# Kernel tuning notes

Measured on AMD Instinct MI355X. Metric: run time of the kernel, lower is better.

## Reference

```python
import jax, jax.numpy as jnp
import numpy as np

NUM_LAYERS = 4
OPTIONS = 32
SHAPE = (3, 32, 32)
D = int(np.prod(SHAPE))  # 3072
H = 256
B = 256


def setup_inputs() -> dict:
    key = jax.random.key(0)
    ks = jax.random.split(key, 4)
    inputs = jax.random.normal(ks[0], (B,) + SHAPE, dtype=jnp.float32)
    Wb = jax.random.normal(ks[1], (D, H), dtype=jnp.float32) * 0.02
    bb = jnp.zeros((H,), dtype=jnp.float32)
    Wo_stack = jax.random.normal(ks[2], (NUM_LAYERS, H, OPTIONS * D), dtype=jnp.float32) * 0.02
    bo_stack = jnp.zeros((NUM_LAYERS, OPTIONS * D), dtype=jnp.float32)
    bias_stack = jnp.zeros((NUM_LAYERS, OPTIONS, D), dtype=jnp.float32)
    return {"inputs": inputs, "Wb": Wb, "bb": bb, "Wo_stack": Wo_stack,
            "bo_stack": bo_stack, "bias_stack": bias_stack}


def reference(inputs, Wb, bb, Wo_stack, bo_stack, bias_stack):
    """Iterative residual vector quantization (VQ-DRAW encoder).

    Returns (encodings [B, num_layers] int32, reconstructions [B, *SHAPE]).
    """
    b = inputs.shape[0]
    x = inputs.reshape(b, D)                      # [B, D] flattened target
    cur = jnp.zeros_like(x)                       # current reconstruction
    encodings = []
    for i in range(NUM_LAYERS):
        base_out = jax.nn.relu(cur @ Wb + bb)                     # [B, H]
        layer_out = (base_out @ Wo_stack[i] + bo_stack[i])        # [B, O*D]
        layer_out = layer_out.reshape(b, OPTIONS, D) + bias_stack[i][None]
        new = cur[:, None, :] + layer_out                          # [B, O, D]
        # per-(example, option) MSE-sum loss, fused argmin over options
        losses = jnp.sum(jnp.square(new - x[:, None, :]), axis=-1)  # [B, O]
        idx = jnp.argmin(losses, axis=-1)                          # [B]
        encodings.append(idx)
        cur = jnp.take_along_axis(new, idx[:, None, None], axis=1)[:, 0]  # [B, D]
    return jnp.stack(encodings, axis=-1), cur.reshape(inputs.shape)
```

## Files before the change

kernel.cpp:

```cpp
#include <hip/hip_runtime.h>
#include <hip/hip_bf16.h>

#define B_ 256
#define D_ 3072
#define H_ 256
#define OPT_ 32
#define OD_ 98304
#define NL_ 4

typedef __attribute__((ext_vector_type(8))) short short8;
typedef __attribute__((ext_vector_type(4))) float f32x4;

__device__ __forceinline__ unsigned short f2bf(float f) {
    unsigned int u = __float_as_uint(f);
    unsigned int r = (u + 0x7FFFu + ((u >> 16) & 1u)) >> 16;
    return (unsigned short)r;
}

__global__ __launch_bounds__(256) void init_kernel(const float* __restrict__ x,
                                                   float* __restrict__ cur,
                                                   float* __restrict__ rx,
                                                   float* __restrict__ zpart) {
    int gid0 = blockIdx.x * 256 + threadIdx.x;
    for (int g = gid0; g < B_ * D_; g += 131072) {
        cur[g] = 0.f;
        rx[g] = -x[g];
    }
    for (int g = gid0; g < 16 * B_ * H_; g += 131072) zpart[g] = 0.f;
}

__global__ __launch_bounds__(256) void gemm1_kernel(const float* __restrict__ cur,
                                                    const float* __restrict__ Wb,
                                                    float* __restrict__ zpart) {
    int t = threadIdx.x;
    int ks = blockIdx.x >> 5;
    int bg = blockIdx.x & 31;
    const float* wp = Wb + (size_t)ks * 192 * H_ + t;
    const float* cp = cur + (size_t)(bg * 8) * D_ + ks * 192;
    float acc[8] = {0.f, 0.f, 0.f, 0.f, 0.f, 0.f, 0.f, 0.f};
#pragma unroll 4
    for (int dd = 0; dd < 192; ++dd) {
        float w = wp[(size_t)dd * H_];
#pragma unroll
        for (int g = 0; g < 8; ++g) acc[g] += cp[(size_t)g * D_ + dd] * w;
    }
#pragma unroll
    for (int g = 0; g < 8; ++g)
        zpart[ks * (B_ * H_) + (bg * 8 + g) * H_ + t] = acc[g];
}

__global__ __launch_bounds__(256) void e_kernel(const float* __restrict__ zpart,
                                                const float* __restrict__ bb,
                                                unsigned char* __restrict__ base_ready,
                                                float* __restrict__ basef) {
    int m = blockIdx.x, k = threadIdx.x;
    float z = bb[k];
#pragma unroll
    for (int ks = 0; ks < 16; ++ks) z += zpart[ks * (B_ * H_) + m * H_ + k];
    z = z > 0.f ? z : 0.f;
    *(unsigned short*)(base_ready + (k >> 5) * 20480 + m * 80 + (k & 31) * 2) = f2bf(z);
    basef[m * H_ + k] = z;
}

__global__ __launch_bounds__(512, 4) void g2_kernel(const unsigned char* __restrict__ base_ready,
                                                    const float* __restrict__ Wo,
                                                    const float* __restrict__ biasL,
                                                    const float* __restrict__ boL,
                                                    const float* __restrict__ rx,
                                                    float* __restrict__ partial) {
    __shared__ __align__(16) unsigned char ldsA[2][20480];
    __shared__ __align__(16) unsigned char ldsW[2][10240];

    int t = threadIdx.x;
    int lane = t & 63, wv = t >> 6;
    int bx = blockIdx.x;
    int ncol0 = bx * 128;
    int o = bx / 24;
    int dbase = (bx % 24) * 128;

    int wm = wv >> 1, wn = wv & 1;
    int lrow = lane & 15, lk = lane >> 4;
    int nW = t & 127, kq = t >> 7;

    f32x4 acc[4][4];
#pragma unroll
    for (int mi = 0; mi < 4; ++mi)
#pragma unroll
        for (int ni = 0; ni < 4; ++ni) acc[mi][ni] = 0.f;

    uint4 pa0, pa1, pa2;
    float wf[8];

#define LOADA(S) { const unsigned char* gA = base_ready + (S) * 20480;           \
    pa0 = *(const uint4*)(gA + t * 16);                                          \
    pa1 = *(const uint4*)(gA + 8192 + t * 16);                                   \
    if (t < 256) pa2 = *(const uint4*)(gA + 16384 + t * 16); }

#define LOADW(S) {                                                               \
    const float* gp0 = Wo + (size_t)((S) * 32 + kq * 4) * OD_ + ncol0 + nW;      \
    wf[0] = gp0[0]; wf[1] = gp0[OD_]; wf[2] = gp0[2 * OD_]; wf[3] = gp0[3 * OD_];\
    const float* gp1 = gp0 + (size_t)16 * OD_;                                   \
    wf[4] = gp1[0]; wf[5] = gp1[OD_]; wf[6] = gp1[2 * OD_]; wf[7] = gp1[3 * OD_]; }

#define WRITEA(BUF) {                                                            \
    *(uint4*)(ldsA[BUF] + t * 16) = pa0;                                         \
    *(uint4*)(ldsA[BUF] + 8192 + t * 16) = pa1;                                  \
    if (t < 256) *(uint4*)(ldsA[BUF] + 16384 + t * 16) = pa2; }

#define WRITEW(BUF) {                                                            \
    uint2 pk0, pk1;                                                              \
    pk0.x = (unsigned)f2bf(wf[0]) | ((unsigned)f2bf(wf[1]) << 16);               \
    pk0.y = (unsigned)f2bf(wf[2]) | ((unsigned)f2bf(wf[3]) << 16);               \
    *(uint2*)(ldsW[BUF] + nW * 80 + kq * 8) = pk0;                               \
    pk1.x = (unsigned)f2bf(wf[4]) | ((unsigned)f2bf(wf[5]) << 16);               \
    pk1.y = (unsigned)f2bf(wf[6]) | ((unsigned)f2bf(wf[7]) << 16);               \
    *(uint2*)(ldsW[BUF] + nW * 80 + 32 + kq * 8) = pk1; }

    LOADA(0); LOADW(0);
    WRITEA(0); WRITEW(0);
    __syncthreads();
    LOADA(1); LOADW(1);

    for (int s = 0; s < 8; ++s) {
        int cur = s & 1;
        short8 bfr[4];
#pragma unroll
        for (int ni = 0; ni < 4; ++ni) {
            int nn = wn * 64 + ni * 16 + lrow;
            bfr[ni] = *(const short8*)(ldsW[cur] + nn * 80 + lk * 16);
        }
#pragma unroll
        for (int mi = 0; mi < 4; ++mi) {
            int row = wm * 64 + mi * 16 + lrow;
            short8 af = *(const short8*)(ldsA[cur] + row * 80 + lk * 16);
#pragma unroll
            for (int ni = 0; ni < 4; ++ni)
                acc[mi][ni] = __builtin_amdgcn_mfma_f32_16x16x32_bf16(af, bfr[ni], acc[mi][ni], 0, 0, 0);
        }
        if (s < 7) { WRITEA(cur ^ 1); WRITEW(cur ^ 1); }
        __syncthreads();
        if (s < 6) { LOADA(s + 2); LOADW(s + 2); }
    }

#undef LOADA
#undef LOADW
#undef WRITEA
#undef WRITEW

    float q[4];
#pragma unroll
    for (int ni = 0; ni < 4; ++ni) {
        int dcol = dbase + wn * 64 + ni * 16 + lrow;
        q[ni] = biasL[o * D_ + dcol] + boL[o * D_ + dcol];
    }
    float ssum[4][4];
#pragma unroll
    for (int mi = 0; mi < 4; ++mi)
#pragma unroll
        for (int r = 0; r < 4; ++r) ssum[mi][r] = 0.f;

#pragma unroll
    for (int mi = 0; mi < 4; ++mi) {
#pragma unroll
        for (int ni = 0; ni < 4; ++ni) {
            int dcol = dbase + wn * 64 + ni * 16 + lrow;
#pragma unroll
            for (int r = 0; r < 4; ++r) {
                int rowm = wm * 64 + mi * 16 + lk * 4 + r;
                float tv = acc[mi][ni][r] + rx[rowm * D_ + dcol] + q[ni];
                ssum[mi][r] += tv * tv;
            }
        }
    }
#pragma unroll
    for (int mi = 0; mi < 4; ++mi)
#pragma unroll
        for (int r = 0; r < 4; ++r) {
            float v = ssum[mi][r];
            v += __shfl_xor(v, 1);
            v += __shfl_xor(v, 2);
            v += __shfl_xor(v, 4);
            v += __shfl_xor(v, 8);
            if (lrow == 0) {
                int rowm = wm * 64 + mi * 16 + lk * 4 + r;
                partial[(rowm * OPT_ + o) * 48 + (bx % 24) * 2 + wn] = v;
            }
        }
}

__global__ __launch_bounds__(256) void c_kernel(const float* __restrict__ partial,
                                                int* __restrict__ idxbuf,
                                                float* __restrict__ enc, int layer) {
    __shared__ float ls[32];
    int b = blockIdx.x, t = threadIdx.x;
    int oo = t >> 3, j8 = t & 7;
    const float* pp = partial + (b * OPT_ + oo) * 48;
    float v = 0.f;
#pragma unroll
    for (int j = 0; j < 6; ++j) v += pp[j8 + 8 * j];
    v += __shfl_xor(v, 1);
    v += __shfl_xor(v, 2);
    v += __shfl_xor(v, 4);
    if (j8 == 0) ls[oo] = v;
    __syncthreads();
    if (t < 32) {
        float mv = ls[t];
        int mi = t;
#pragma unroll
        for (int m = 16; m >= 1; m >>= 1) {
            float ov = __shfl_xor(mv, m);
            int oi = __shfl_xor(mi, m);
            if (ov < mv || (ov == mv && oi < mi)) { mv = ov; mi = oi; }
        }
        if (t == 0) {
            idxbuf[b] = mi;
            enc[b * NL_ + layer] = (float)mi;
        }
    }
}

__global__ __launch_bounds__(256) void bucket_kernel(const int* __restrict__ idxbuf,
                                                     int* __restrict__ ocount,
                                                     int* __restrict__ olist,
                                                     int* __restrict__ work) {
    __shared__ int lcnt[32];
    int t = threadIdx.x;
    if (t < 32) lcnt[t] = 0;
    __syncthreads();
    int o = idxbuf[t];
    int pos = atomicAdd(&lcnt[o], 1);
    olist[o * 256 + pos] = t;
    __syncthreads();
    if (t < 32) ocount[t] = lcnt[t];
    if (t == 0) {
        int n = 0;
        for (int oo = 0; oo < 32; ++oo) {
            int c = lcnt[oo];
            for (int ch = 0; ch * 8 < c; ++ch) work[n++] = (oo << 8) | ch;
        }
        work[63] = n;
    }
}

__global__ __launch_bounds__(256) void d_kernel(const int* __restrict__ work,
                                                const int* __restrict__ ocount,
                                                const int* __restrict__ olist,
                                                const float* __restrict__ basef,
                                                const float* __restrict__ Wo,
                                                const float* __restrict__ boL,
                                                const float* __restrict__ biasL,
                                                const float* __restrict__ x,
                                                float* __restrict__ cur,
                                                float* __restrict__ rx) {
    __shared__ float basL[8][256];
    int t = threadIdx.x;
    int dt = blockIdx.y;
    int nit = work[63];

    for (int j = blockIdx.x; j < nit; j += 32) {
        int wi = work[j];
        int o = wi >> 8;
        int c0 = (wi & 255) * 8;
        int cnt = ocount[o];
        int rem = cnt - c0;
        if (rem > 8) rem = 8;

        int bidx[8];
#pragma unroll
        for (int g = 0; g < 8; ++g) {
            int idx = c0 + g;
            if (idx >= cnt) idx = cnt - 1;
            bidx[g] = olist[o * 256 + idx];
        }
        __syncthreads();
#pragma unroll
        for (int g = 0; g < 8; ++g) basL[g][t] = basef[bidx[g] * H_ + t];
        __syncthreads();

        int d = dt * 256 + t;
        const float* wp = Wo + (size_t)o * D_ + d;
        size_t nn = (size_t)o * D_ + d;
        float bov = boL[nn];
        float biv = biasL[nn];

        float acc[8] = {0.f, 0.f, 0.f, 0.f, 0.f, 0.f, 0.f, 0.f};
        for (int k0 = 0; k0 < 256; k0 += 8) {
            float w[8];
#pragma unroll
            for (int u = 0; u < 8; ++u) w[u] = wp[(size_t)(k0 + u) * OD_];
#pragma unroll
            for (int h = 0; h < 2; ++h) {
                int kb = k0 + h * 4;
                f32x4 bv[8];
#pragma unroll
                for (int g = 0; g < 8; ++g) bv[g] = *(const f32x4*)&basL[g][kb];
#pragma unroll
                for (int u = 0; u < 4; ++u) {
                    float wu = w[h * 4 + u];
#pragma unroll
                    for (int g = 0; g < 8; ++g) acc[g] += bv[g][u] * wu;
                }
            }
        }
#pragma unroll
        for (int g = 0; g < 8; ++g) {
            if (g < rem) {
                int b = bidx[g];
                float outv = cur[b * D_ + d] + acc[g] + bov + biv;
                cur[b * D_ + d] = outv;
                rx[b * D_ + d] = outv - x[b * D_ + d];
            }
        }
    }
}

extern "C" void kernel_launch(void* const* d_in, const int* in_sizes, int n_in,
                              void* d_out, int out_size, void* d_ws, size_t ws_size,
                              hipStream_t stream) {
    const float* x    = (const float*)d_in[0];
    const float* Wb   = (const float*)d_in[1];
    const float* bb   = (const float*)d_in[2];
    const float* Wo   = (const float*)d_in[3];
    const float* bo   = (const float*)d_in[4];
    const float* bias = (const float*)d_in[5];

    float* out = (float*)d_out;
    float* enc = out;
    float* cur = out + 1024;

    float* ws = (float*)d_ws;
    float* zpart   = ws;
    float* partial = ws + 1048576;
    float* rx      = ws + 1441792;
    float* basef   = ws + 2228224;
    unsigned char* base_ready = (unsigned char*)(ws + 2293760);
    int* idxbuf    = (int*)(ws + 2334720);
    int* ocount    = (int*)(ws + 2334976);
    int* olist     = (int*)(ws + 2335008);
    int* work      = (int*)(ws + 2343200);

    init_kernel<<<512, 256, 0, stream>>>(x, cur, rx, zpart);

    for (int i = 0; i < NL_; ++i) {
        const float* WoL   = Wo + (size_t)i * H_ * OD_;
        const float* boLp  = bo + (size_t)i * OD_;
        const float* biasL = bias + (size_t)i * OD_;
        if (i > 0) gemm1_kernel<<<512, 256, 0, stream>>>(cur, Wb, zpart);
        e_kernel<<<256, 256, 0, stream>>>(zpart, bb, base_ready, basef);
        g2_kernel<<<768, 512, 0, stream>>>(base_ready, WoL, biasL, boLp, rx, partial);
        c_kernel<<<256, 256, 0, stream>>>(partial, idxbuf, enc, i);
        bucket_kernel<<<1, 256, 0, stream>>>(idxbuf, ocount, olist, work);
        d_kernel<<<dim3(32, 12), 256, 0, stream>>>(work, ocount, olist, basef, WoL, boLp, biasL, x, cur, rx);
    }
}
```

Baseline: 419.0 us.

## Use global_load_lds DMA in g2 pipeline and fold bucketing into d_kernel

The g2 GEMM now loads the A tile straight into LDS with global_load_lds instead of staging it through registers. It also double-buffers the W prefetch two stages ahead and uses explicit waitcnt/barrier placement, so loads overlap MFMA work. Separately, bucket_kernel is removed: each d_kernel block recomputes option counts and ranks from idxbuf in shared memory, saving one launch per layer. The cost is redundant bucketing work in every d block, extra syncs, and more reliance on hand-written waitcnt counts being correct.

Result: slower. 460.9 us (+10.0%).

```diff
diff --git a/kernel.cpp b/kernel.cpp
--- a/kernel.cpp
+++ b/kernel.cpp
@@ -88,41 +88,55 @@
 #pragma unroll
         for (int ni = 0; ni < 4; ++ni) acc[mi][ni] = 0.f;
 
-    uint4 pa0, pa1, pa2;
-    float wf[8];
-
-#define LOADA(S) { const unsigned char* gA = base_ready + (S) * 20480;           \
-    pa0 = *(const uint4*)(gA + t * 16);                                          \
-    pa1 = *(const uint4*)(gA + 8192 + t * 16);                                   \
-    if (t < 256) pa2 = *(const uint4*)(gA + 16384 + t * 16); }
-
-#define LOADW(S) {                                                               \
-    const float* gp0 = Wo + (size_t)((S) * 32 + kq * 4) * OD_ + ncol0 + nW;      \
-    wf[0] = gp0[0]; wf[1] = gp0[OD_]; wf[2] = gp0[2 * OD_]; wf[3] = gp0[3 * OD_];\
-    const float* gp1 = gp0 + (size_t)16 * OD_;                                   \
-    wf[4] = gp1[0]; wf[5] = gp1[OD_]; wf[6] = gp1[2 * OD_]; wf[7] = gp1[3 * OD_]; }
-
-#define WRITEA(BUF) {                                                            \
-    *(uint4*)(ldsA[BUF] + t * 16) = pa0;                                         \
-    *(uint4*)(ldsA[BUF] + 8192 + t * 16) = pa1;                                  \
-    if (t < 256) *(uint4*)(ldsA[BUF] + 16384 + t * 16) = pa2; }
-
-#define WRITEW(BUF) {                                                            \
-    uint2 pk0, pk1;                                                              \
-    pk0.x = (unsigned)f2bf(wf[0]) | ((unsigned)f2bf(wf[1]) << 16);               \
-    pk0.y = (unsigned)f2bf(wf[2]) | ((unsigned)f2bf(wf[3]) << 16);               \
-    *(uint2*)(ldsW[BUF] + nW * 80 + kq * 8) = pk0;                               \
-    pk1.x = (unsigned)f2bf(wf[4]) | ((unsigned)f2bf(wf[5]) << 16);               \
-    pk1.y = (unsigned)f2bf(wf[6]) | ((unsigned)f2bf(wf[7]) << 16);               \
+    float wfX[8], wfY[8];
+
+#define DMA_A(S, BUF) {                                                                  \
+    const unsigned char* gA = base_ready + (S) * 20480;                                  \
+    __builtin_amdgcn_global_load_lds(                                                    \
+        (const __attribute__((address_space(1))) unsigned int*)(gA + t * 16),            \
+        (__attribute__((address_space(3))) unsigned int*)(&ldsA[BUF][0] + wv * 1024),    \
+        16, 0, 0);                                                                       \
+    __builtin_amdgcn_global_load_lds(                                                    \
+        (const __attribute__((address_space(1))) unsigned int*)(gA + 8192 + t * 16),     \
+        (__attribute__((address_space(3))) unsigned int*)(&ldsA[BUF][0] + 8192 + wv * 1024), \
+        16, 0, 0);                                                                       \
+    if (wv < 4)                                                                          \
+        __builtin_amdgcn_global_load_lds(                                                \
+            (const __attribute__((address_space(1))) unsigned int*)(gA + 16384 + t * 16),\
+            (__attribute__((address_space(3))) unsigned int*)(&ldsA[BUF][0] + 16384 + wv * 1024), \
+            16, 0, 0); }
+
+#define LOADW_(S, WF) {                                                                  \
+    const float* gp0 = Wo + (size_t)((S) * 32 + kq * 4) * OD_ + ncol0 + nW;              \
+    WF[0] = gp0[0]; WF[1] = gp0[OD_]; WF[2] = gp0[2 * OD_]; WF[3] = gp0[3 * OD_];        \
+    const float* gp1 = gp0 + (size_t)16 * OD_;                                           \
+    WF[4] = gp1[0]; WF[5] = gp1[OD_]; WF[6] = gp1[2 * OD_]; WF[7] = gp1[3 * OD_]; }
+
+#define WRITEW_(BUF, WF) {                                                               \
+    uint2 pk0, pk1;                                                                      \
+    pk0.x = (unsigned)f2bf(WF[0]) | ((unsigned)f2bf(WF[1]) << 16);                       \
+    pk0.y = (unsigned)f2bf(WF[2]) | ((unsigned)f2bf(WF[3]) << 16);                       \
+    *(uint2*)(ldsW[BUF] + nW * 80 + kq * 8) = pk0;                                       \
+    pk1.x = (unsigned)f2bf(WF[4]) | ((unsigned)f2bf(WF[5]) << 16);                       \
+    pk1.y = (unsigned)f2bf(WF[6]) | ((unsigned)f2bf(WF[7]) << 16);                       \
     *(uint2*)(ldsW[BUF] + nW * 80 + 32 + kq * 8) = pk1; }
 
-    LOADA(0); LOADW(0);
-    WRITEA(0); WRITEW(0);
-    __syncthreads();
-    LOADA(1); LOADW(1);
-
+    DMA_A(0, 0);
+    LOADW_(0, wfX);
+    LOADW_(1, wfY);
+    WRITEW_(0, wfX);
+    asm volatile("s_waitcnt lgkmcnt(0)" ::: "memory");
+    __builtin_amdgcn_s_barrier();
+    __builtin_amdgcn_sched_barrier(0);
+
+#pragma unroll
     for (int s = 0; s < 8; ++s) {
         int cur = s & 1;
+        if (s < 7) DMA_A(s + 1, cur ^ 1);
+        if (s < 6) {
+            if ((s & 1) == 0) { LOADW_(s + 2, wfX); }
+            else              { LOADW_(s + 2, wfY); }
+        }
         short8 bfr[4];
 #pragma unroll
         for (int ni = 0; ni < 4; ++ni) {
@@ -137,15 +151,19 @@
             for (int ni = 0; ni < 4; ++ni)
                 acc[mi][ni] = __builtin_amdgcn_mfma_f32_16x16x32_bf16(af, bfr[ni], acc[mi][ni], 0, 0, 0);
         }
-        if (s < 7) { WRITEA(cur ^ 1); WRITEW(cur ^ 1); }
-        __syncthreads();
-        if (s < 6) { LOADA(s + 2); LOADW(s + 2); }
-    }
-
-#undef LOADA
-#undef LOADW
-#undef WRITEA
-#undef WRITEW
+        if (s < 7) {
+            if ((s & 1) == 0) { WRITEW_(cur ^ 1, wfY); }
+            else              { WRITEW_(cur ^ 1, wfX); }
+            if (s < 6) asm volatile("s_waitcnt vmcnt(8) lgkmcnt(0)" ::: "memory");
+            else       asm volatile("s_waitcnt vmcnt(0) lgkmcnt(0)" ::: "memory");
+            __builtin_amdgcn_s_barrier();
+            __builtin_amdgcn_sched_barrier(0);
+        }
+    }
+
+#undef DMA_A
+#undef LOADW_
+#undef WRITEW_
 
     float q[4];
 #pragma unroll
@@ -219,32 +237,7 @@
     }
 }
 
-__global__ __launch_bounds__(256) void bucket_kernel(const int* __restrict__ idxbuf,
-                                                     int* __restrict__ ocount,
-                                                     int* __restrict__ olist,
-                                                     int* __restrict__ work) {
-    __shared__ int lcnt[32];
-    int t = threadIdx.x;
-    if (t < 32) lcnt[t] = 0;
-    __syncthreads();
-    int o = idxbuf[t];
-    int pos = atomicAdd(&lcnt[o], 1);
-    olist[o * 256 + pos] = t;
-    __syncthreads();
-    if (t < 32) ocount[t] = lcnt[t];
-    if (t == 0) {
-        int n = 0;
-        for (int oo = 0; oo < 32; ++oo) {
-            int c = lcnt[oo];
-            for (int ch = 0; ch * 8 < c; ++ch) work[n++] = (oo << 8) | ch;
-        }
-        work[63] = n;
-    }
-}
-
-__global__ __launch_bounds__(256) void d_kernel(const int* __restrict__ work,
-                                                const int* __restrict__ ocount,
-                                                const int* __restrict__ olist,
+__global__ __launch_bounds__(256) void d_kernel(const int* __restrict__ idxbuf,
                                                 const float* __restrict__ basef,
                                                 const float* __restrict__ Wo,
                                                 const float* __restrict__ boL,
@@ -252,27 +245,47 @@
                                                 const float* __restrict__ x,
                                                 float* __restrict__ cur,
                                                 float* __restrict__ rx) {
+    __shared__ int sidx[256];
+    __shared__ int scnt[32];
+    __shared__ int snch[32];
+    __shared__ int chunk_b[8];
     __shared__ float basL[8][256];
     int t = threadIdx.x;
     int dt = blockIdx.y;
-    int nit = work[63];
-
-    for (int j = blockIdx.x; j < nit; j += 32) {
-        int wi = work[j];
-        int o = wi >> 8;
-        int c0 = (wi & 255) * 8;
-        int cnt = ocount[o];
+
+    sidx[t] = idxbuf[t];
+    __syncthreads();
+    if (t < 32) {
+        int c = 0;
+        for (int b = 0; b < 256; ++b) c += (sidx[b] == t);
+        scnt[t] = c;
+        snch[t] = (c + 7) >> 3;
+    }
+    __syncthreads();
+    int myo = sidx[t];
+    int myrank = 0;
+    for (int b = 0; b < t; ++b) myrank += (sidx[b] == myo);
+
+    for (int j = blockIdx.x; ; j += 32) {
+        int o = -1, ch = 0, pre = 0;
+        for (int oo = 0; oo < 32; ++oo) {
+            int n = snch[oo];
+            if (j < pre + n) { o = oo; ch = j - pre; break; }
+            pre += n;
+        }
+        if (o < 0) break;
+        int cnt = scnt[o];
+        int c0 = ch * 8;
         int rem = cnt - c0;
         if (rem > 8) rem = 8;
 
+        __syncthreads();
+        if (myo == o && myrank >= c0 && myrank < c0 + 8) chunk_b[myrank - c0] = t;
+        __syncthreads();
+
         int bidx[8];
 #pragma unroll
-        for (int g = 0; g < 8; ++g) {
-            int idx = c0 + g;
-            if (idx >= cnt) idx = cnt - 1;
-            bidx[g] = olist[o * 256 + idx];
-        }
-        __syncthreads();
+        for (int g = 0; g < 8; ++g) bidx[g] = chunk_b[(g < rem) ? g : (rem - 1)];
 #pragma unroll
         for (int g = 0; g < 8; ++g) basL[g][t] = basef[bidx[g] * H_ + t];
         __syncthreads();
@@ -335,9 +348,6 @@
     float* basef   = ws + 2228224;
     unsigned char* base_ready = (unsigned char*)(ws + 2293760);
     int* idxbuf    = (int*)(ws + 2334720);
-    int* ocount    = (int*)(ws + 2334976);
-    int* olist     = (int*)(ws + 2335008);
-    int* work      = (int*)(ws + 2343200);
 
     init_kernel<<<512, 256, 0, stream>>>(x, cur, rx, zpart);
 
@@ -349,7 +359,6 @@
         e_kernel<<<256, 256, 0, stream>>>(zpart, bb, base_ready, basef);
         g2_kernel<<<768, 512, 0, stream>>>(base_ready, WoL, biasL, boLp, rx, partial);
         c_kernel<<<256, 256, 0, stream>>>(partial, idxbuf, enc, i);
-        bucket_kernel<<<1, 256, 0, stream>>>(idxbuf, ocount, olist, work);
-        d_kernel<<<dim3(32, 12), 256, 0, stream>>>(work, ocount, olist, basef, WoL, boLp, biasL, x, cur, rx);
-    }
-}
+        d_kernel<<<dim3(32, 12), 256, 0, stream>>>(idxbuf, basef, WoL, boLp, biasL, x, cur, rx);
+    }
+}
```
